# Kernel tuning notes

Measured on AMD Instinct MI355X. Metric: run time of the kernel, lower is better.

The kernel has to match this reference:

```python
import jax, jax.numpy as jnp
import numpy as np
from jax import lax

DN = ('NHWC', 'HWIO', 'NHWC')
OUTPUT_STRIDE = 2
PEAK_THRESHOLD = 0.2


def setup_inputs() -> dict:
    key = jax.random.key(0)
    k1, k2, k3 = jax.random.split(key, 3)
    crops = jax.random.normal(k1, (128, 192, 192, 1), dtype=jnp.float32)
    # simple confmap backbone: stride-2 conv -> relu -> 3x3 conv to 17 nodes
    W1 = jax.random.normal(k2, (3, 3, 1, 32), dtype=jnp.float32) * 0.1
    b1 = jnp.zeros((32,), dtype=jnp.float32)
    W2 = jax.random.normal(k3, (3, 3, 32, 17), dtype=jnp.float32) * 0.1
    b2 = jnp.zeros((17,), dtype=jnp.float32)
    return {"crops": crops, "W1": W1, "b1": b1, "W2": W2, "b2": b2}


def _confmaps(crops, W1, b1, W2, b2):
    # keras_model forward: (B, 192, 192, 1) -> (B, 96, 96, 17), output_stride = 2
    h = lax.conv_general_dilated(crops, W1, (2, 2), 'SAME', dimension_numbers=DN) + b1
    h = jax.nn.relu(h)
    cms = lax.conv_general_dilated(h, W2, (1, 1), 'SAME', dimension_numbers=DN) + b2
    return cms


def _find_global_peaks_local(cms, threshold):
    # cms: (B, H, W, N) -> peaks (B, N, 2) in (x, y), vals (B, N)
    B, H, W, N = cms.shape
    cm = jnp.transpose(cms, (0, 3, 1, 2)).reshape(B, N, H * W)  # (B, N, HW)
    flat_idx = jnp.argmax(cm, axis=-1)                           # (B, N)
    vals = jnp.take_along_axis(cm, flat_idx[..., None], axis=-1)[..., 0]
    yi = flat_idx // W
    xi = flat_idx % W

    def gather(yy, xx):
        yy = jnp.clip(yy, 0, H - 1)
        xx = jnp.clip(xx, 0, W - 1)
        return jnp.take_along_axis(cm, (yy * W + xx)[..., None], axis=-1)[..., 0]

    # quarter-pixel local gradient offset (refinement='local')
    dx = 0.25 * jnp.sign(gather(yi, xi + 1) - gather(yi, xi - 1))
    dy = 0.25 * jnp.sign(gather(yi + 1, xi) - gather(yi - 1, xi))

    pts = jnp.stack([xi.astype(cm.dtype) + dx, yi.astype(cm.dtype) + dy], axis=-1)
    pts = jnp.where(vals[..., None] >= threshold, pts, jnp.nan)
    return pts, vals


def reference(crops, W1, b1, W2, b2):
    # preprocess: inputs already float grayscale, input_scale=1.0 -> identity
    cms = _confmaps(crops, W1, b1, W2, b2)
    peak_points, peak_vals = _find_global_peaks_local(cms, PEAK_THRESHOLD)
    peak_points = peak_points * OUTPUT_STRIDE  # adjust to input image grid
    # pack (x, y, val) into one array: (B, nodes, 3)
    return jnp.concatenate([peak_points, peak_vals[..., None]], axis=-1)
```

## Files before the change

kernel.cpp:

```cpp
#include <hip/hip_runtime.h>


#define NCH 17
#define C1 32
#define TW 24
#define TH 32
#define HT_W 26
#define HT_H 34
#define HSTR 28
#define IN_W 53
#define IN_H 69
#define NG 32
#define NHPX (HT_H * HT_W)
#define SH_PLANE (HT_H * HSTR)

__device__ __forceinline__ unsigned long long pack_key(float v, unsigned flat) {
    unsigned ub = __float_as_uint(v);
    ub = (ub & 0x80000000u) ? ~ub : (ub | 0x80000000u);
    return ((unsigned long long)ub << 32) | (unsigned)(~flat);
}

__device__ __forceinline__ void conv1_ch(
    const float* __restrict__ W1g, const float* __restrict__ b1g,
    const float* s_in, float* dst, int c, int t, int ty0, int tx0) {
    const float bias = b1g[c];
    float w1[9];
#pragma unroll
    for (int q = 0; q < 9; ++q) w1[q] = W1g[q * C1 + c];
#pragma unroll
    for (int i = 0; i < 4; ++i) {
        int p = t + i * 256;
        if (i < 3 || p < NHPX) {
            int r = p / HT_W, cc = p - r * HT_W;
            int hy = ty0 - 1 + r, hx = tx0 - 1 + cc;
            float vf = (hy >= 0 && hy < 96 && hx >= 0 && hx < 96) ? 1.f : 0.f;
            const float* ip = s_in + 2 * r * IN_W + 2 * cc;
            float a = bias;
#pragma unroll
            for (int qy = 0; qy < 3; ++qy)
#pragma unroll
                for (int qx = 0; qx < 3; ++qx)
                    a = fmaf(ip[qy * IN_W + qx], w1[qy * 3 + qx], a);
            dst[r * HSTR + cc] = fmaxf(a, 0.f) * vf;
        }
    }
}

__global__ __launch_bounds__(256, 6) void conv_peaks_kernel(
    const float* __restrict__ crops, const float* __restrict__ W1g,
    const float* __restrict__ b1g, const float* __restrict__ W2g,
    const float* __restrict__ b2g, unsigned long long* __restrict__ peaks) {
    __shared__ __align__(16) float s_in[IN_H * IN_W];
    __shared__ __align__(16) float s_h[2][SH_PLANE];

    const int t = threadIdx.x;
    const int b = blockIdx.y;
    const int ty0 = (blockIdx.x >> 2) * TH;
    const int tx0 = (blockIdx.x & 3) * TW;
    const int iy0 = 2 * ty0 - 2;
    const int ix0 = 2 * tx0 - 2;
    const float* cb = crops + b * 192 * 192;

    for (int p = t; p < IN_H * IN_W; p += 256) {
        int r = p / IN_W, cc = p - r * IN_W;
        int iy = iy0 + r, ix = ix0 + cc;
        float v = 0.f;
        if (iy >= 0 && ix >= 0 && iy < 192 && ix < 192) v = cb[iy * 192 + ix];
        s_in[p] = v;
    }
    __syncthreads();
    conv1_ch(W1g, b1g, s_in, s_h[0], 0, t, ty0, tx0);

    const int ly = t >> 3;
    const int lx0 = (t & 7) * 3;
    float acc[NCH][3];
#pragma unroll
    for (int n = 0; n < NCH; ++n)
#pragma unroll
        for (int p = 0; p < 3; ++p) acc[n][p] = 0.f;

#pragma unroll 1
    for (int g = 0; g < NG; ++g) {
        __syncthreads();

        if (g < NG - 1)
            conv1_ch(W1g, b1g, s_in, s_h[(g + 1) & 1], g + 1, t, ty0, tx0);

        {
            const float* hp = s_h[g & 1] + ly * HSTR + lx0;
            float hr[3][5];
#pragma unroll
            for (int ky = 0; ky < 3; ++ky)
#pragma unroll
                for (int j = 0; j < 5; ++j) hr[ky][j] = hp[ky * HSTR + j];
#pragma unroll
            for (int k = 0; k < 9; ++k) {
                const int ky = k / 3, kx = k - ky * 3;
                const float* wb = W2g + (k * C1 + g) * NCH;
                float w[NCH];
#pragma unroll
                for (int n = 0; n < NCH; ++n) w[n] = wb[n];
#pragma unroll
                for (int p = 0; p < 3; ++p) {
                    const float h = hr[ky][kx + p];
#pragma unroll
                    for (int n = 0; n < NCH; ++n)
                        acc[n][p] = fmaf(h, w[n], acc[n][p]);
                }
            }
        }
    }

    const int yg = ty0 + ly, xg = tx0 + lx0;
    const int lane = t & 63;
#pragma unroll
    for (int n = 0; n < NCH; ++n) {
        const float bb = b2g[n];
        unsigned long long pk = pack_key(acc[n][0] + bb, (unsigned)(yg * 96 + xg));
#pragma unroll
        for (int p = 1; p < 3; ++p) {
            unsigned long long o = pack_key(acc[n][p] + bb, (unsigned)(yg * 96 + xg + p));
            if (o > pk) pk = o;
        }
#pragma unroll
        for (int off = 32; off; off >>= 1) {
            unsigned long long o = __shfl_down(pk, off, 64);
            if (o > pk) pk = o;
        }
        if (lane == 0) atomicMax(&peaks[b * NCH + n], pk);
    }
}

__global__ __launch_bounds__(64) void refine_kernel(
    const float* __restrict__ crops, const float* __restrict__ W1g,
    const float* __restrict__ b1g, const float* __restrict__ W2g,
    const unsigned long long* __restrict__ peaks, float* __restrict__ out) {
    const int bn = blockIdx.x;
    const int b = bn / NCH, n = bn % NCH;
    const int lane = threadIdx.x;

    unsigned long long pk = peaks[bn];
    unsigned key = (unsigned)(pk >> 32);
    unsigned fbits = (key & 0x80000000u) ? (key ^ 0x80000000u) : ~key;
    float val = __uint_as_float(fbits);
    int flat = (int)(~(unsigned)(pk & 0xffffffffu));
    int yi = flat / 96, xi = flat - yi * 96;

    const int j = lane >> 4;
    int yy = yi + ((j == 2) ? 1 : 0) - ((j == 3) ? 1 : 0);
    int xx = xi + ((j == 0) ? 1 : 0) - ((j == 1) ? 1 : 0);
    yy = min(max(yy, 0), 95);
    xx = min(max(xx, 0), 95);

    const float* cb = crops + b * 192 * 192;
    float pat[7][7];
#pragma unroll
    for (int r = 0; r < 7; ++r) {
        int iy = 2 * yy - 2 + r;
#pragma unroll
        for (int s = 0; s < 7; ++s) {
            int ix = 2 * xx - 2 + s;
            pat[r][s] = (iy >= 0 && iy < 192 && ix >= 0 && ix < 192)
                            ? cb[iy * 192 + ix] : 0.f;
        }
    }

    float part = 0.f;
#pragma unroll
    for (int ci = 0; ci < 2; ++ci) {
        const int c = (lane & 15) + ci * 16;
        const float bias = b1g[c];
        float w1[9];
#pragma unroll
        for (int q = 0; q < 9; ++q) w1[q] = W1g[q * C1 + c];
#pragma unroll
        for (int dy = 0; dy < 3; ++dy) {
#pragma unroll
            for (int dx = 0; dx < 3; ++dx) {
                int hy = yy - 1 + dy, hx = xx - 1 + dx;
                if (hy >= 0 && hy < 96 && hx >= 0 && hx < 96) {
                    float a = bias;
#pragma unroll
                    for (int qy = 0; qy < 3; ++qy)
#pragma unroll
                        for (int qx = 0; qx < 3; ++qx)
                            a = fmaf(pat[2 * dy + qy][2 * dx + qx],
                                     w1[qy * 3 + qx], a);
                    float hval = fmaxf(a, 0.f);
                    part = fmaf(hval, W2g[((dy * 3 + dx) * C1 + c) * NCH + n], part);
                }
            }
        }
    }
    for (int off = 8; off; off >>= 1) part += __shfl_down(part, off, 16);
    float g0 = __shfl(part, 0, 64);
    float g1 = __shfl(part, 16, 64);
    float g2 = __shfl(part, 32, 64);
    float g3 = __shfl(part, 48, 64);

    if (lane == 0) {
        float d0 = g0 - g1, d1 = g2 - g3;
        float sx = (d0 > 0.f) ? 1.f : ((d0 < 0.f) ? -1.f : 0.f);
        float sy = (d1 > 0.f) ? 1.f : ((d1 < 0.f) ? -1.f : 0.f);
        float px = ((float)xi + 0.25f * sx) * 2.f;
        float py = ((float)yi + 0.25f * sy) * 2.f;
        if (!(val >= 0.2f)) {
            px = __int_as_float(0x7fc00000);
            py = __int_as_float(0x7fc00000);
        }
        out[bn * 3 + 0] = px;
        out[bn * 3 + 1] = py;
        out[bn * 3 + 2] = val;
    }
}

extern "C" void kernel_launch(void* const* d_in, const int* in_sizes, int n_in,
                              void* d_out, int out_size, void* d_ws, size_t ws_size,
                              hipStream_t stream) {
    const float* crops = (const float*)d_in[0];
    const float* W1 = (const float*)d_in[1];
    const float* b1 = (const float*)d_in[2];
    const float* W2 = (const float*)d_in[3];
    const float* b2 = (const float*)d_in[4];
    float* out = (float*)d_out;
    unsigned long long* peaks = (unsigned long long*)d_ws;

    hipMemsetAsync(d_ws, 0, 128 * NCH * sizeof(unsigned long long), stream);

    dim3 gridB(12, 128);
    conv_peaks_kernel<<<gridB, 256, 0, stream>>>(crops, W1, b1, W2, b2, peaks);
    refine_kernel<<<128 * NCH, 64, 0, stream>>>(crops, W1, b1, W2, peaks, out);
}
```

Before: 246.6 us.

## Batch first-conv channels into groups of eight to cut barriers

```diff
diff --git a/kernel.cpp b/kernel.cpp
--- a/kernel.cpp
+++ b/kernel.cpp
@@ -10,7 +10,8 @@
 #define HSTR 28
 #define IN_W 53
 #define IN_H 69
-#define NG 32
+#define CG 8
+#define NG 4
 #define NHPX (HT_H * HT_W)
 #define SH_PLANE (HT_H * HSTR)
 
@@ -20,38 +21,12 @@
     return ((unsigned long long)ub << 32) | (unsigned)(~flat);
 }
 
-__device__ __forceinline__ void conv1_ch(
-    const float* __restrict__ W1g, const float* __restrict__ b1g,
-    const float* s_in, float* dst, int c, int t, int ty0, int tx0) {
-    const float bias = b1g[c];
-    float w1[9];
-#pragma unroll
-    for (int q = 0; q < 9; ++q) w1[q] = W1g[q * C1 + c];
-#pragma unroll
-    for (int i = 0; i < 4; ++i) {
-        int p = t + i * 256;
-        if (i < 3 || p < NHPX) {
-            int r = p / HT_W, cc = p - r * HT_W;
-            int hy = ty0 - 1 + r, hx = tx0 - 1 + cc;
-            float vf = (hy >= 0 && hy < 96 && hx >= 0 && hx < 96) ? 1.f : 0.f;
-            const float* ip = s_in + 2 * r * IN_W + 2 * cc;
-            float a = bias;
-#pragma unroll
-            for (int qy = 0; qy < 3; ++qy)
-#pragma unroll
-                for (int qx = 0; qx < 3; ++qx)
-                    a = fmaf(ip[qy * IN_W + qx], w1[qy * 3 + qx], a);
-            dst[r * HSTR + cc] = fmaxf(a, 0.f) * vf;
-        }
-    }
-}
-
-__global__ __launch_bounds__(256, 6) void conv_peaks_kernel(
+__global__ __launch_bounds__(256, 3) void conv_peaks_kernel(
     const float* __restrict__ crops, const float* __restrict__ W1g,
     const float* __restrict__ b1g, const float* __restrict__ W2g,
     const float* __restrict__ b2g, unsigned long long* __restrict__ peaks) {
     __shared__ __align__(16) float s_in[IN_H * IN_W];
-    __shared__ __align__(16) float s_h[2][SH_PLANE];
+    __shared__ __align__(16) float s_h[CG * SH_PLANE];
 
     const int t = threadIdx.x;
     const int b = blockIdx.y;
@@ -68,8 +43,6 @@
         if (iy >= 0 && ix >= 0 && iy < 192 && ix < 192) v = cb[iy * 192 + ix];
         s_in[p] = v;
     }
-    __syncthreads();
-    conv1_ch(W1g, b1g, s_in, s_h[0], 0, t, ty0, tx0);
 
     const int ly = t >> 3;
     const int lx0 = (t & 7) * 3;
@@ -83,20 +56,46 @@
     for (int g = 0; g < NG; ++g) {
         __syncthreads();
 
-        if (g < NG - 1)
-            conv1_ch(W1g, b1g, s_in, s_h[(g + 1) & 1], g + 1, t, ty0, tx0);
-
-        {
-            const float* hp = s_h[g & 1] + ly * HSTR + lx0;
+#pragma unroll
+        for (int i = 0; i < 4; ++i) {
+            int p = t + i * 256;
+            if (i < 3 || t < NHPX - 768) {
+                int r = p / HT_W, cc = p - r * HT_W;
+                int hy = ty0 - 1 + r, hx = tx0 - 1 + cc;
+                float vf = (hy >= 0 && hy < 96 && hx >= 0 && hx < 96) ? 1.f : 0.f;
+                const float* ip = s_in + 2 * r * IN_W + 2 * cc;
+                float in9[9];
+#pragma unroll
+                for (int qy = 0; qy < 3; ++qy)
+#pragma unroll
+                    for (int qx = 0; qx < 3; ++qx)
+                        in9[qy * 3 + qx] = ip[qy * IN_W + qx];
+#pragma unroll
+                for (int cl = 0; cl < CG; ++cl) {
+                    const int c = g * CG + cl;
+                    float a = b1g[c];
+#pragma unroll
+                    for (int q = 0; q < 9; ++q)
+                        a = fmaf(in9[q], W1g[q * C1 + c], a);
+                    s_h[cl * SH_PLANE + r * HSTR + cc] = fmaxf(a, 0.f) * vf;
+                }
+            }
+        }
+        __syncthreads();
+
+#pragma unroll 1
+        for (int cl = 0; cl < CG; ++cl) {
+            const float* hp = s_h + cl * SH_PLANE + ly * HSTR + lx0;
             float hr[3][5];
 #pragma unroll
             for (int ky = 0; ky < 3; ++ky)
 #pragma unroll
                 for (int j = 0; j < 5; ++j) hr[ky][j] = hp[ky * HSTR + j];
+            const int c = g * CG + cl;
 #pragma unroll
             for (int k = 0; k < 9; ++k) {
                 const int ky = k / 3, kx = k - ky * 3;
-                const float* wb = W2g + (k * C1 + g) * NCH;
+                const float* wb = W2g + (k * C1 + c) * NCH;
                 float w[NCH];
 #pragma unroll
                 for (int n = 0; n < NCH; ++n) w[n] = wb[n];
```

After: 227.2 us. 7.9% less time.
